# Kernel tuning notes

Measured on AMD Instinct MI355X. Metric: run time of the kernel, lower is better.

## Reference

```python
import jax, jax.numpy as jnp
import numpy as np

BS, IN, HID, LAT, OUT = 8192, 48, 256, 64, 128
CAT = LAT + OUT + HID  # LSTM input size = 448


def setup_inputs() -> dict:
    key = jax.random.key(0)
    ks = jax.random.split(key, 13)
    s = 0.02
    return {
        "x": jax.random.normal(ks[0], (BS, IN), jnp.float32),
        "enc": jax.random.normal(ks[1], (BS, HID), jnp.float32),
        "z": jax.random.normal(ks[2], (BS, LAT), jnp.float32),
        "W_ih": jax.random.normal(ks[3], (4 * OUT, CAT), jnp.float32) * s,
        "W_hh": jax.random.normal(ks[4], (4 * OUT, OUT), jnp.float32) * s,
        "b_ih": jax.random.normal(ks[5], (4 * OUT,), jnp.float32) * s,
        "b_hh": jax.random.normal(ks[6], (4 * OUT,), jnp.float32) * s,
        "W_u0": jax.random.normal(ks[7], (OUT, IN), jnp.float32) * s,
        "b_u0": jax.random.normal(ks[8], (OUT,), jnp.float32) * s,
        "W_h1": jax.random.normal(ks[9], (OUT, CAT), jnp.float32) * s,
        "b_h1": jax.random.normal(ks[10], (OUT,), jnp.float32) * s,
        "W_h2": jax.random.normal(ks[11], (OUT, CAT), jnp.float32) * s,
        "b_h2": jax.random.normal(ks[12], (OUT,), jnp.float32) * s,
        "horizon": 50,
    }


def reference(x, enc, z, W_ih, W_hh, b_ih, b_hh, W_u0, b_u0, W_h1, b_h1, W_h2, b_h2, horizon):
    # initial input u0 = Linear(input_size -> output_size)(x)
    u0 = x @ W_u0.T + b_u0                       # [bs, OUT]
    xi0 = jnp.concatenate([z, u0, enc], axis=-1)  # [bs, CAT]
    h0 = xi0 @ W_h1.T + b_h1                     # LSTM hidden init [bs, OUT]
    c0 = xi0 @ W_h2.T + b_h2                     # LSTM cell init   [bs, OUT]
    b = b_ih + b_hh

    def step(carry, _):
        h, c, yi = carry
        xi = jnp.concatenate([z, yi, enc], axis=-1)   # [bs, CAT]
        gates = xi @ W_ih.T + h @ W_hh.T + b          # [bs, 4*OUT]
        i_g, f_g, g_g, o_g = jnp.split(gates, 4, axis=-1)  # torch order: i,f,g,o
        c_new = jax.nn.sigmoid(f_g) * c + jax.nn.sigmoid(i_g) * jnp.tanh(g_g)
        h_new = jax.nn.sigmoid(o_g) * jnp.tanh(c_new)
        return (h_new, c_new, h_new), h_new

    _, ys = jax.lax.scan(step, (h0, c0, u0), None, length=horizon)  # [T, bs, OUT]
    # torch stacks yi [bs, 1, OUT] along dim=1 -> [bs, T, 1, OUT]
    return jnp.transpose(ys, (1, 0, 2))[:, :, None, :]
```

## Files before the change

### kernel.cpp

```cpp
#include <hip/hip_runtime.h>
#include <stdint.h>

typedef short bf16x8 __attribute__((ext_vector_type(8)));
typedef float f32x4 __attribute__((ext_vector_type(4)));

#define MFMA16(a,b,c) __builtin_amdgcn_mfma_f32_16x16x32_bf16((a),(b),(c),0,0,0)

__device__ __forceinline__ unsigned short bf16_rne(float f){
  unsigned int u = __builtin_bit_cast(unsigned int, f);
  return (unsigned short)((u + 0x7FFFu + ((u>>16)&1u)) >> 16);
}
__device__ __forceinline__ float bf16_f(unsigned short h){
  unsigned int u = ((unsigned int)h) << 16;
  return __builtin_bit_cast(float, u);
}

#define SZ_WINIT (48*24*512*2)
#define OFF_W0   (SZ_WINIT)
#define SZ_W0    (32*12*512*2)
#define OFF_WC   (OFF_W0 + SZ_W0)
#define SZ_WC    (32*8*512*2)
#define OFF_BIAS (OFF_WC + SZ_WC)

__device__ __forceinline__ void pack_split(unsigned short* __restrict__ base, int KT, int n, int k, float v){
  int nt = n>>4, n16 = n&15, kt = k>>5, kr = k&31;
  int lane = n16 + ((kr>>3)<<4), j = kr&7;
  unsigned short hi = bf16_rne(v);
  unsigned short lo = bf16_rne(v - bf16_f(hi));
  base[((nt*2*KT + kt)*64 + lane)*8 + j] = hi;
  base[((nt*2*KT + KT + kt)*64 + lane)*8 + j] = lo;
}

__global__ void decoder_prep(const float* __restrict__ W_ih, const float* __restrict__ W_hh,
                             const float* __restrict__ b_ih, const float* __restrict__ b_hh,
                             const float* __restrict__ W_u0, const float* __restrict__ b_u0,
                             const float* __restrict__ W_h1, const float* __restrict__ b_h1,
                             const float* __restrict__ W_h2, const float* __restrict__ b_h2,
                             unsigned short* __restrict__ wsu, float* __restrict__ bias_out){
  int idx = blockIdx.x*256 + threadIdx.x;
  if (idx < 768*384) {
    int n = idx/384, k = idx - n*384;
    float v = 0.f;
    if (n < 256) {
      const float* W = (n<128) ? (W_h1 + n*448) : (W_h2 + (n-128)*448);
      if (k < 64) v = W[k];
      else if (k < 320) v = W[192 + k - 64];
      else if (k < 368) { float s = 0.f; int j = k-320;
        for (int c=0;c<128;++c) s += W[64+c]*W_u0[c*48+j];
        v = s; }
    } else {
      int m = n-256;
      if (k < 64) v = W_ih[m*448 + k];
      else if (k < 320) v = W_ih[m*448 + 192 + k - 64];
    }
    pack_split(wsu, 12, n, k, v);
    return;
  }
  idx -= 768*384;
  if (idx < 512*192) {
    int n = idx/192, k = idx - n*192;
    float v = 0.f;
    if (k < 48)      { float s=0.f; for (int c=0;c<128;++c) s += W_ih[n*448+64+c]*W_u0[c*48+k]; v = s; }
    else if (k == 48){ float s=0.f; for (int c=0;c<128;++c) s += W_ih[n*448+64+c]*b_u0[c];      v = s; }
    else if (k >= 64)  v = W_hh[n*128 + k - 64];
    pack_split(wsu + OFF_W0/2, 6, n, k, v);
    return;
  }
  idx -= 512*192;
  if (idx < 512*128) {
    int n = idx>>7, k = idx&127;
    float v = W_ih[n*448 + 64 + k] + W_hh[n*128 + k];
    pack_split(wsu + OFF_WC/2, 4, n, k, v);
    return;
  }
  idx -= 512*128;
  if (idx < 768) {
    float v;
    if (idx < 256) {
      const float* W  = (idx<128) ? (W_h1 + idx*448) : (W_h2 + (idx-128)*448);
      float s = (idx<128) ? b_h1[idx] : b_h2[idx-128];
      for (int c=0;c<128;++c) s += W[64+c]*b_u0[c];
      v = s;
    } else v = b_ih[idx-256] + b_hh[idx-256];
    bias_out[idx] = v;
  }
}


__global__ __launch_bounds__(512, 2)
void decoder_main(const float* __restrict__ x, const float* __restrict__ enc, const float* __restrict__ z,
                  const unsigned short* __restrict__ wsu, const float* __restrict__ bias_init,
                  const int* __restrict__ hz, float* __restrict__ out){
  extern __shared__ char smem[];
  unsigned short* a0_hi = (unsigned short*)(smem);
  unsigned short* a0_lo = (unsigned short*)(smem + 12800);
  unsigned short* xi_hi = (unsigned short*)(smem + 25600);
  unsigned short* xi_lo = (unsigned short*)(smem + 50688);
  unsigned short* hbh   = (unsigned short*)(smem + 25600);
  unsigned short* hbl   = (unsigned short*)(smem + 43008);
  float*          c0l   = (float*)(smem + 60416);

  const int tid = threadIdx.x;
  const int w = tid>>6, lane = tid&63, n16 = lane&15, p = lane>>4;
  const int R0 = blockIdx.x*32;
  const int T = hz[0];

  for (int i = tid; i < 32*384; i += 512) {
    int r = i/384, c = i - r*384;
    float v;
    if (c < 64)       v = z[(R0+r)*64 + c];
    else if (c < 320) v = enc[(R0+r)*256 + c - 64];
    else if (c < 368) v = x[(R0+r)*48 + c - 320];
    else              v = 0.f;
    unsigned short hi = bf16_rne(v);
    xi_hi[r*392 + c] = hi;
    xi_lo[r*392 + c] = bf16_rne(v - bf16_f(hi));
  }
  for (int i = tid; i < 32*64; i += 512) {
    int r = i>>6, c = i&63;
    float v = (c<48) ? x[(R0+r)*48 + c] : (c==48 ? 1.f : 0.f);
    unsigned short hi = bf16_rne(v);
    a0_hi[r*200 + c] = hi;
    a0_lo[r*200 + c] = bf16_rne(v - bf16_f(hi));
  }
  __syncthreads();

  const bf16x8* WIp = (const bf16x8*)wsu;
  f32x4 accs[6][2];
  #pragma unroll
  for (int i=0;i<6;++i){
    int nt = (i<2) ? (2*w+i) : (16 + 8*(i-2) + w);
    float b = bias_init[nt*16 + n16];
    accs[i][0] = (f32x4){b,b,b,b};
    accs[i][1] = accs[i][0];
  }
  for (int kt=0; kt<12; ++kt) {
    bf16x8 ah0 = *(const bf16x8*)(xi_hi +      n16 *392 + kt*32 + p*8);
    bf16x8 ah1 = *(const bf16x8*)(xi_hi + (16+n16)*392 + kt*32 + p*8);
    bf16x8 al0 = *(const bf16x8*)(xi_lo +      n16 *392 + kt*32 + p*8);
    bf16x8 al1 = *(const bf16x8*)(xi_lo + (16+n16)*392 + kt*32 + p*8);
    #pragma unroll
    for (int i=0;i<6;++i){
      int nt = (i<2) ? (2*w+i) : (16 + 8*(i-2) + w);
      const bf16x8* fp = WIp + ((unsigned)(nt*24 + kt))*64 + lane;
      bf16x8 bh = fp[0];
      bf16x8 bl = fp[12*64];
      accs[i][0] = MFMA16(ah0, bh, accs[i][0]);
      accs[i][1] = MFMA16(ah1, bh, accs[i][1]);
      accs[i][0] = MFMA16(al0, bh, accs[i][0]);
      accs[i][1] = MFMA16(al1, bh, accs[i][1]);
      accs[i][0] = MFMA16(ah0, bl, accs[i][0]);
      accs[i][1] = MFMA16(ah1, bl, accs[i][1]);
    }
  }
  __syncthreads();

  #pragma unroll
  for (int i=0;i<2;++i){
    int ntg = 2*w + i;
    #pragma unroll
    for (int mt=0;mt<2;++mt){
      #pragma unroll
      for (int e=0;e<4;++e){
        int row = mt*16 + p*4 + e;
        float v = accs[i][mt][e];
        if (ntg < 8) {
          int col = 64 + ntg*16 + n16;
          unsigned short hi = bf16_rne(v);
          a0_hi[row*200 + col] = hi;
          a0_lo[row*200 + col] = bf16_rne(v - bf16_f(hi));
        } else {
          c0l[row*128 + (ntg-8)*16 + n16] = v;
        }
      }
    }
  }
  __syncthreads();

  f32x4 creg[2];
  #pragma unroll
  for (int mt=0;mt<2;++mt)
    #pragma unroll
    for (int e=0;e<4;++e)
      creg[mt][e] = c0l[(mt*16 + p*4 + e)*128 + w*16 + n16];

  f32x4 base_r[2][4];
  #pragma unroll
  for (int q=0;q<4;++q)
    #pragma unroll
    for (int mt=0;mt<2;++mt)
      base_r[mt][q] = accs[2+q][mt];

  const bf16x8* WCp = (const bf16x8*)(wsu + OFF_WC/2);
  bf16x8 wchi[4][4], wclo[4][4];
  #pragma unroll
  for (int q=0;q<4;++q){
    int nt = 8*q + w;
    #pragma unroll
    for (int kt=0;kt<4;++kt){
      wchi[q][kt] = WCp[((unsigned)(nt*8 + kt))*64 + lane];
      wclo[q][kt] = WCp[((unsigned)(nt*8 + 4 + kt))*64 + lane];
    }
  }

  unsigned rt[2][4];
  #pragma unroll
  for (int mt=0;mt<2;++mt)
    #pragma unroll
    for (int e=0;e<4;++e)
      rt[mt][e] = (unsigned)(R0 + mt*16 + p*4 + e)*(unsigned)(T*128) + (unsigned)(w*16 + n16);

  f32x4 acc[2][4];
  const float K1 = 1.44269504088896340736f;
  const float K2 = 2.88539008177792681472f;

  auto lstm_tail = [&](int t, int wb){
    #pragma unroll
    for (int mt=0;mt<2;++mt){
      #pragma unroll
      for (int e=0;e<4;++e){
        float iv = acc[mt][0][e], fv = acc[mt][1][e], gv = acc[mt][2][e], ov = acc[mt][3][e];
        float c = creg[mt][e];
        float ef = __builtin_amdgcn_exp2f(-K1*fv);
        float sf = __builtin_amdgcn_rcpf(1.f + ef);
        float ei = __builtin_amdgcn_exp2f(-K1*iv);
        float eg = __builtin_amdgcn_exp2f(-K2*gv);
        float d  = __builtin_amdgcn_rcpf((1.f+ei)*(1.f+eg));
        c = sf*c + (1.f-eg)*d;
        float eo = __builtin_amdgcn_exp2f(-K1*ov);
        float ec = __builtin_amdgcn_exp2f(-K2*c);
        float h  = (1.f-ec)*__builtin_amdgcn_rcpf((1.f+eo)*(1.f+ec));
        creg[mt][e] = c;
        out[rt[mt][e] + (unsigned)(t*128)] = h;
        int row = mt*16 + p*4 + e;
        unsigned short hh = bf16_rne(h);
        hbh[wb*4352 + row*136 + w*16 + n16] = hh;
        hbl[wb*4352 + row*136 + w*16 + n16] = bf16_rne(h - bf16_f(hh));
      }
    }
  };

  {
    const bf16x8* W0p = (const bf16x8*)(wsu + OFF_W0/2);
    #pragma unroll
    for (int kt=0;kt<6;++kt){
      bf16x8 ah0 = *(const bf16x8*)(a0_hi +      n16 *200 + kt*32 + p*8);
      bf16x8 ah1 = *(const bf16x8*)(a0_hi + (16+n16)*200 + kt*32 + p*8);
      bf16x8 al0 = *(const bf16x8*)(a0_lo +      n16 *200 + kt*32 + p*8);
      bf16x8 al1 = *(const bf16x8*)(a0_lo + (16+n16)*200 + kt*32 + p*8);
      #pragma unroll
      for (int q=0;q<4;++q){
        const bf16x8* fp = W0p + ((unsigned)((8*q+w)*12 + kt))*64 + lane;
        bf16x8 bh = fp[0];
        bf16x8 bl = fp[6*64];
        #pragma unroll
        for (int mt=0;mt<2;++mt){
          bf16x8 ah = mt ? ah1 : ah0;
          bf16x8 al = mt ? al1 : al0;
          f32x4 ci = (kt==0) ? base_r[mt][q] : acc[mt][q];
          ci = MFMA16(ah, bh, ci);
          ci = MFMA16(al, bh, ci);
          ci = MFMA16(ah, bl, ci);
          acc[mt][q] = ci;
        }
      }
    }
    lstm_tail(0, 0);
  }
  __syncthreads();

  for (int t=1; t<T; ++t){
    const int rb = (t-1)&1, wb = t&1;
    const unsigned short* hr = hbh + rb*4352;
    const unsigned short* lr = hbl + rb*4352;
    #pragma unroll
    for (int kt=0;kt<4;++kt){
      bf16x8 ah0 = *(const bf16x8*)(hr +      n16 *136 + kt*32 + p*8);
      bf16x8 ah1 = *(const bf16x8*)(hr + (16+n16)*136 + kt*32 + p*8);
      bf16x8 al0 = *(const bf16x8*)(lr +      n16 *136 + kt*32 + p*8);
      bf16x8 al1 = *(const bf16x8*)(lr + (16+n16)*136 + kt*32 + p*8);
      #pragma unroll
      for (int q=0;q<4;++q){
        #pragma unroll
        for (int mt=0;mt<2;++mt){
          bf16x8 ah = mt ? ah1 : ah0;
          bf16x8 al = mt ? al1 : al0;
          f32x4 ci = (kt==0) ? base_r[mt][q] : acc[mt][q];
          ci = MFMA16(ah, wchi[q][kt], ci);
          ci = MFMA16(al, wchi[q][kt], ci);
          ci = MFMA16(ah, wclo[q][kt], ci);
          acc[mt][q] = ci;
        }
      }
    }
    lstm_tail(t, wb);
    __syncthreads();
  }
}

extern "C" void kernel_launch(void* const* d_in, const int* in_sizes, int n_in,
                              void* d_out, int out_size, void* d_ws, size_t ws_size,
                              hipStream_t stream) {
    (void)in_sizes; (void)n_in; (void)out_size; (void)ws_size;
    const float* x    = (const float*)d_in[0];
    const float* enc  = (const float*)d_in[1];
    const float* z    = (const float*)d_in[2];
    const float* W_ih = (const float*)d_in[3];
    const float* W_hh = (const float*)d_in[4];
    const float* b_ih = (const float*)d_in[5];
    const float* b_hh = (const float*)d_in[6];
    const float* W_u0 = (const float*)d_in[7];
    const float* b_u0 = (const float*)d_in[8];
    const float* W_h1 = (const float*)d_in[9];
    const float* b_h1 = (const float*)d_in[10];
    const float* W_h2 = (const float*)d_in[11];
    const float* b_h2 = (const float*)d_in[12];
    const int*   hz   = (const int*)d_in[13];
    float* out = (float*)d_out;
    unsigned short* wsu = (unsigned short*)d_ws;
    float* bias = (float*)((char*)d_ws + OFF_BIAS);

    (void)hipFuncSetAttribute((const void*)decoder_main,
                              hipFuncAttributeMaxDynamicSharedMemorySize, 76800);

    decoder_prep<<<dim3(1795), dim3(256), 0, stream>>>(W_ih, W_hh, b_ih, b_hh, W_u0, b_u0,
                                                       W_h1, b_h1, W_h2, b_h2, wsu, bias);
    decoder_main<<<dim3(256), dim3(512), 76800, stream>>>(x, enc, z, wsu, bias, hz, out);
}
```

Before: 380.0 us.

## Rewrite weight prep into compose+pack kernels and swizzle LDS in decoder

Splits the weight preparation into a kernel that computes the W_u0 compositions once per row block using shared memory, and a pack kernel that writes full 8-element bf16 vectors per lane instead of scattered scalars. The main kernel swaps MFMA operand roles so the weights become the A operand, which lets the init results stay in registers (c0 and h0 written directly, no LDS round-trip for c0). It also adds XOR-swizzled LDS layouts to avoid bank conflicts, skips zero-padded k-tiles for the recurrent gate slices in the init GEMM, and emits vectorized f32x4 output stores one step later. This is many changes at once: it touches the prep cost, the LDS traffic, and the global store pattern, and the new index math carries some risk of errors.

```diff
diff --git a/kernel.cpp b/kernel.cpp
--- a/kernel.cpp
+++ b/kernel.cpp
@@ -3,6 +3,7 @@
 
 typedef short bf16x8 __attribute__((ext_vector_type(8)));
 typedef float f32x4 __attribute__((ext_vector_type(4)));
+typedef unsigned short u16x4 __attribute__((ext_vector_type(4)));
 
 #define MFMA16(a,b,c) __builtin_amdgcn_mfma_f32_16x16x32_bf16((a),(b),(c),0,0,0)
 
@@ -21,206 +22,240 @@
 #define OFF_WC   (OFF_W0 + SZ_W0)
 #define SZ_WC    (32*8*512*2)
 #define OFF_BIAS (OFF_WC + SZ_WC)
-
-__device__ __forceinline__ void pack_split(unsigned short* __restrict__ base, int KT, int n, int k, float v){
-  int nt = n>>4, n16 = n&15, kt = k>>5, kr = k&31;
-  int lane = n16 + ((kr>>3)<<4), j = kr&7;
-  unsigned short hi = bf16_rne(v);
-  unsigned short lo = bf16_rne(v - bf16_f(hi));
-  base[((nt*2*KT + kt)*64 + lane)*8 + j] = hi;
-  base[((nt*2*KT + KT + kt)*64 + lane)*8 + j] = lo;
-}
-
-__global__ void decoder_prep(const float* __restrict__ W_ih, const float* __restrict__ W_hh,
-                             const float* __restrict__ b_ih, const float* __restrict__ b_hh,
-                             const float* __restrict__ W_u0, const float* __restrict__ b_u0,
-                             const float* __restrict__ W_h1, const float* __restrict__ b_h1,
-                             const float* __restrict__ W_h2, const float* __restrict__ b_h2,
-                             unsigned short* __restrict__ wsu, float* __restrict__ bias_out){
-  int idx = blockIdx.x*256 + threadIdx.x;
-  if (idx < 768*384) {
-    int n = idx/384, k = idx - n*384;
-    float v = 0.f;
-    if (n < 256) {
-      const float* W = (n<128) ? (W_h1 + n*448) : (W_h2 + (n-128)*448);
-      if (k < 64) v = W[k];
-      else if (k < 320) v = W[192 + k - 64];
-      else if (k < 368) { float s = 0.f; int j = k-320;
-        for (int c=0;c<128;++c) s += W[64+c]*W_u0[c*48+j];
-        v = s; }
-    } else {
-      int m = n-256;
-      if (k < 64) v = W_ih[m*448 + k];
-      else if (k < 320) v = W_ih[m*448 + 192 + k - 64];
-    }
-    pack_split(wsu, 12, n, k, v);
+#define OFF_XQ   (OFF_BIAS + 4096)
+#define OFF_XH   (OFF_XQ + 512*49*4)
+
+__global__ __launch_bounds__(256)
+void decoder_compose(const float* __restrict__ W_ih, const float* __restrict__ W_u0,
+                     const float* __restrict__ b_u0, const float* __restrict__ W_h1,
+                     const float* __restrict__ W_h2, float* __restrict__ ws){
+  __shared__ float wu[128][49];
+  __shared__ float wrow[16][128];
+  float* Xq = (float*)((char*)ws + OFF_XQ);
+  float* Xh = (float*)((char*)ws + OFF_XH);
+  const int b = blockIdx.x, tid = threadIdx.x;
+  for (int i = tid; i < 128*49; i += 256){
+    int c = i/49, j = i - c*49;
+    wu[c][j] = (j < 48) ? W_u0[c*48 + j] : b_u0[c];
+  }
+  for (int i = tid; i < 16*128; i += 256){
+    int r = i>>7, c = i&127;
+    const float* src;
+    if (b < 32) src = W_ih + (b*16 + r)*448 + 64;
+    else { int mm = (b-32)*16 + r; src = (mm<128) ? (W_h1 + mm*448 + 64) : (W_h2 + (mm-128)*448 + 64); }
+    wrow[r][c] = src[c];
+  }
+  __syncthreads();
+  for (int o = tid; o < 16*49; o += 256){
+    int r = o/49, j = o - r*49;
+    float s = 0.f;
+    #pragma unroll 8
+    for (int c = 0; c < 128; ++c) s += wrow[r][c]*wu[c][j];
+    if (b < 32) Xq[(b*16+r)*49 + j] = s;
+    else        Xh[((b-32)*16+r)*49 + j] = s;
+  }
+}
+
+__global__ __launch_bounds__(256)
+void decoder_pack(const float* __restrict__ W_ih, const float* __restrict__ W_hh,
+                  const float* __restrict__ b_ih, const float* __restrict__ b_hh,
+                  const float* __restrict__ W_h1, const float* __restrict__ W_h2,
+                  const float* __restrict__ b_h1, const float* __restrict__ b_h2,
+                  unsigned short* __restrict__ wsu, float* __restrict__ ws){
+  const float* Xq = (const float*)((const char*)ws + OFF_XQ);
+  const float* Xh = (const float*)((const char*)ws + OFF_XH);
+  float* bias = (float*)((char*)ws + OFF_BIAS);
+  const int gid = blockIdx.x*256 + threadIdx.x;
+  const int slot = gid >> 6, lane = gid & 63;
+  const int n16 = lane & 15, p = lane >> 4;
+
+  float v[8];
+  unsigned short* dh; unsigned short* dl;
+  if (slot < 576) {
+    int nt = slot/12, kt = slot - nt*12;
+    int n = nt*16 + n16;
+    #pragma unroll
+    for (int j=0;j<8;++j){
+      int k = kt*32 + p*8 + j;
+      float xv = 0.f;
+      if (n < 256) {
+        const float* W = (n<128) ? (W_h1 + n*448) : (W_h2 + (n-128)*448);
+        if (k < 64) xv = W[k];
+        else if (k < 320) xv = W[192 + k - 64];
+        else if (k < 368) xv = Xh[n*49 + (k-320)];
+      } else {
+        int m = n - 256;
+        if (k < 64) xv = W_ih[m*448 + k];
+        else if (k < 320) xv = W_ih[m*448 + 192 + k - 64];
+      }
+      v[j] = xv;
+    }
+    dh = wsu + ((nt*24 + kt)*64 + lane)*8;
+    dl = wsu + ((nt*24 + 12 + kt)*64 + lane)*8;
+  } else if (slot < 768) {
+    int s2 = slot - 576;
+    int nt = s2/6, kt = s2 - nt*6;
+    int n = nt*16 + n16;
+    #pragma unroll
+    for (int j=0;j<8;++j){
+      int k = kt*32 + p*8 + j;
+      float xv = 0.f;
+      if (k < 49)      xv = Xq[n*49 + k];
+      else if (k >= 64) xv = W_hh[n*128 + k - 64];
+      v[j] = xv;
+    }
+    unsigned short* b = wsu + OFF_W0/2;
+    dh = b + ((nt*12 + kt)*64 + lane)*8;
+    dl = b + ((nt*12 + 6 + kt)*64 + lane)*8;
+  } else if (slot < 896) {
+    int s3 = slot - 768;
+    int nt = s3>>2, kt = s3&3;
+    int n = nt*16 + n16;
+    #pragma unroll
+    for (int j=0;j<8;++j){
+      int k = kt*32 + p*8 + j;
+      v[j] = W_ih[n*448 + 64 + k] + W_hh[n*128 + k];
+    }
+    unsigned short* b = wsu + OFF_WC/2;
+    dh = b + ((nt*8 + kt)*64 + lane)*8;
+    dl = b + ((nt*8 + 4 + kt)*64 + lane)*8;
+  } else {
+    int i = gid - 896*64;
+    if (i < 768) {
+      float bv;
+      if (i < 128)      bv = b_h1[i] + Xh[i*49 + 48];
+      else if (i < 256) bv = b_h2[i-128] + Xh[i*49 + 48];
+      else              bv = b_ih[i-256] + b_hh[i-256];
+      bias[i] = bv;
+    }
     return;
   }
-  idx -= 768*384;
-  if (idx < 512*192) {
-    int n = idx/192, k = idx - n*192;
-    float v = 0.f;
-    if (k < 48)      { float s=0.f; for (int c=0;c<128;++c) s += W_ih[n*448+64+c]*W_u0[c*48+k]; v = s; }
-    else if (k == 48){ float s=0.f; for (int c=0;c<128;++c) s += W_ih[n*448+64+c]*b_u0[c];      v = s; }
-    else if (k >= 64)  v = W_hh[n*128 + k - 64];
-    pack_split(wsu + OFF_W0/2, 6, n, k, v);
-    return;
-  }
-  idx -= 512*192;
-  if (idx < 512*128) {
-    int n = idx>>7, k = idx&127;
-    float v = W_ih[n*448 + 64 + k] + W_hh[n*128 + k];
-    pack_split(wsu + OFF_WC/2, 4, n, k, v);
-    return;
-  }
-  idx -= 512*128;
-  if (idx < 768) {
-    float v;
-    if (idx < 256) {
-      const float* W  = (idx<128) ? (W_h1 + idx*448) : (W_h2 + (idx-128)*448);
-      float s = (idx<128) ? b_h1[idx] : b_h2[idx-128];
-      for (int c=0;c<128;++c) s += W[64+c]*b_u0[c];
-      v = s;
-    } else v = b_ih[idx-256] + b_hh[idx-256];
-    bias_out[idx] = v;
-  }
-}
-
+  bf16x8 vh, vl;
+  #pragma unroll
+  for (int j=0;j<8;++j){
+    unsigned short h = bf16_rne(v[j]);
+    vh[j] = (short)h;
+    vl[j] = (short)bf16_rne(v[j] - bf16_f(h));
+  }
+  *(bf16x8*)dh = vh;
+  *(bf16x8*)dl = vl;
+}
+
+#define LDS_A0H 0
+#define LDS_A0L 12288
+#define LDS_XIH 24576
+#define LDS_XIL 49152
+#define LDS_H   24576
+#define LDS_TOTAL 73728
 
 __global__ __launch_bounds__(512, 2)
 void decoder_main(const float* __restrict__ x, const float* __restrict__ enc, const float* __restrict__ z,
-                  const unsigned short* __restrict__ wsu, const float* __restrict__ bias_init,
+                  const unsigned short* __restrict__ wsu, const float* __restrict__ bias,
                   const int* __restrict__ hz, float* __restrict__ out){
   extern __shared__ char smem[];
-  unsigned short* a0_hi = (unsigned short*)(smem);
-  unsigned short* a0_lo = (unsigned short*)(smem + 12800);
-  unsigned short* xi_hi = (unsigned short*)(smem + 25600);
-  unsigned short* xi_lo = (unsigned short*)(smem + 50688);
-  unsigned short* hbh   = (unsigned short*)(smem + 25600);
-  unsigned short* hbl   = (unsigned short*)(smem + 43008);
-  float*          c0l   = (float*)(smem + 60416);
-
   const int tid = threadIdx.x;
   const int w = tid>>6, lane = tid&63, n16 = lane&15, p = lane>>4;
+  const int p16 = p*16;
   const int R0 = blockIdx.x*32;
   const int T = hz[0];
 
-  for (int i = tid; i < 32*384; i += 512) {
+  for (int i = tid; i < 32*384; i += 512){
     int r = i/384, c = i - r*384;
     float v;
     if (c < 64)       v = z[(R0+r)*64 + c];
     else if (c < 320) v = enc[(R0+r)*256 + c - 64];
     else if (c < 368) v = x[(R0+r)*48 + c - 320];
     else              v = 0.f;
-    unsigned short hi = bf16_rne(v);
-    xi_hi[r*392 + c] = hi;
-    xi_lo[r*392 + c] = bf16_rne(v - bf16_f(hi));
-  }
-  for (int i = tid; i < 32*64; i += 512) {
+    unsigned short h = bf16_rne(v);
+    int off = r*768 + ((2*c) ^ ((r&7)<<4));
+    *(unsigned short*)(smem + LDS_XIH + off) = h;
+    *(unsigned short*)(smem + LDS_XIL + off) = bf16_rne(v - bf16_f(h));
+  }
+  for (int i = tid; i < 32*64; i += 512){
     int r = i>>6, c = i&63;
-    float v = (c<48) ? x[(R0+r)*48 + c] : (c==48 ? 1.f : 0.f);
-    unsigned short hi = bf16_rne(v);
-    a0_hi[r*200 + c] = hi;
-    a0_lo[r*200 + c] = bf16_rne(v - bf16_f(hi));
-  }
-  __syncthreads();
-
-  const bf16x8* WIp = (const bf16x8*)wsu;
+    float v = (c < 48) ? x[(R0+r)*48 + c] : (c == 48 ? 1.f : 0.f);
+    unsigned short h = bf16_rne(v);
+    int off = r*384 + ((2*c) ^ ((r&7)<<4));
+    *(unsigned short*)(smem + LDS_A0H + off) = h;
+    *(unsigned short*)(smem + LDS_A0L + off) = bf16_rne(v - bf16_f(h));
+  }
+  __syncthreads();
+
+  const int row0 = n16, row1 = 16 + n16;
+  const int s0 = (row0&7)<<4, s1 = (row1&7)<<4;
+
   f32x4 accs[6][2];
   #pragma unroll
   for (int i=0;i<6;++i){
-    int nt = (i<2) ? (2*w+i) : (16 + 8*(i-2) + w);
-    float b = bias_init[nt*16 + n16];
-    accs[i][0] = (f32x4){b,b,b,b};
-    accs[i][1] = accs[i][0];
-  }
-  for (int kt=0; kt<12; ++kt) {
-    bf16x8 ah0 = *(const bf16x8*)(xi_hi +      n16 *392 + kt*32 + p*8);
-    bf16x8 ah1 = *(const bf16x8*)(xi_hi + (16+n16)*392 + kt*32 + p*8);
-    bf16x8 al0 = *(const bf16x8*)(xi_lo +      n16 *392 + kt*32 + p*8);
-    bf16x8 al1 = *(const bf16x8*)(xi_lo + (16+n16)*392 + kt*32 + p*8);
+    int nt = (i==0) ? w : (i==1) ? (8+w) : (16 + 8*(i-2) + w);
+    f32x4 bv = *(const f32x4*)(bias + nt*16 + p*4);
+    accs[i][0] = bv; accs[i][1] = bv;
+  }
+  #pragma unroll
+  for (int kt=0; kt<12; ++kt){
+    bf16x8 bh0 = *(const bf16x8*)(smem + LDS_XIH + row0*768 + ((kt*64 + p16) ^ s0));
+    bf16x8 bh1 = *(const bf16x8*)(smem + LDS_XIH + row1*768 + ((kt*64 + p16) ^ s1));
+    bf16x8 bl0 = *(const bf16x8*)(smem + LDS_XIL + row0*768 + ((kt*64 + p16) ^ s0));
+    bf16x8 bl1 = *(const bf16x8*)(smem + LDS_XIL + row1*768 + ((kt*64 + p16) ^ s1));
+    bf16x8 wa[6], wl[6];
     #pragma unroll
     for (int i=0;i<6;++i){
-      int nt = (i<2) ? (2*w+i) : (16 + 8*(i-2) + w);
-      const bf16x8* fp = WIp + ((unsigned)(nt*24 + kt))*64 + lane;
-      bf16x8 bh = fp[0];
-      bf16x8 bl = fp[12*64];
-      accs[i][0] = MFMA16(ah0, bh, accs[i][0]);
-      accs[i][1] = MFMA16(ah1, bh, accs[i][1]);
-      accs[i][0] = MFMA16(al0, bh, accs[i][0]);
-      accs[i][1] = MFMA16(al1, bh, accs[i][1]);
-      accs[i][0] = MFMA16(ah0, bl, accs[i][0]);
-      accs[i][1] = MFMA16(ah1, bl, accs[i][1]);
-    }
-  }
-  __syncthreads();
-
-  #pragma unroll
-  for (int i=0;i<2;++i){
-    int ntg = 2*w + i;
-    #pragma unroll
-    for (int mt=0;mt<2;++mt){
-      #pragma unroll
-      for (int e=0;e<4;++e){
-        int row = mt*16 + p*4 + e;
-        float v = accs[i][mt][e];
-        if (ntg < 8) {
-          int col = 64 + ntg*16 + n16;
-          unsigned short hi = bf16_rne(v);
-          a0_hi[row*200 + col] = hi;
-          a0_lo[row*200 + col] = bf16_rne(v - bf16_f(hi));
-        } else {
-          c0l[row*128 + (ntg-8)*16 + n16] = v;
-        }
-      }
-    }
-  }
-  __syncthreads();
-
-  f32x4 creg[2];
-  #pragma unroll
-  for (int mt=0;mt<2;++mt)
-    #pragma unroll
-    for (int e=0;e<4;++e)
-      creg[mt][e] = c0l[(mt*16 + p*4 + e)*128 + w*16 + n16];
-
+      if (kt >= 10 && i >= 2) continue;
+      int nt = (i==0) ? w : (i==1) ? (8+w) : (16 + 8*(i-2) + w);
+      wa[i] = *(const bf16x8*)(wsu + ((nt*24 + kt)*64 + lane)*8);
+      wl[i] = *(const bf16x8*)(wsu + ((nt*24 + 12 + kt)*64 + lane)*8);
+    }
+    #pragma unroll
+    for (int i=0;i<6;++i){ if (kt >= 10 && i >= 2) continue;
+      accs[i][0] = MFMA16(wa[i], bh0, accs[i][0]);
+      accs[i][1] = MFMA16(wa[i], bh1, accs[i][1]); }
+    #pragma unroll
+    for (int i=0;i<6;++i){ if (kt >= 10 && i >= 2) continue;
+      accs[i][0] = MFMA16(wa[i], bl0, accs[i][0]);
+      accs[i][1] = MFMA16(wa[i], bl1, accs[i][1]); }
+    #pragma unroll
+    for (int i=0;i<6;++i){ if (kt >= 10 && i >= 2) continue;
+      accs[i][0] = MFMA16(wl[i], bh0, accs[i][0]);
+      accs[i][1] = MFMA16(wl[i], bh1, accs[i][1]); }
+  }
+  __syncthreads();
+
+  #pragma unroll
+  for (int bt=0; bt<2; ++bt){
+    int row = bt*16 + n16, s = (row&7)<<4;
+    u16x4 vh, vl;
+    #pragma unroll
+    for (int e=0;e<4;++e){
+      float hv = accs[0][bt][e];
+      unsigned short h = bf16_rne(hv);
+      vh[e] = h; vl[e] = bf16_rne(hv - bf16_f(h));
+    }
+    int off = row*384 + ((128 + 32*w + 8*p) ^ s);
+    *(u16x4*)(smem + LDS_A0H + off) = vh;
+    *(u16x4*)(smem + LDS_A0L + off) = vl;
+  }
+  f32x4 creg[2] = { accs[1][0], accs[1][1] };
   f32x4 base_r[2][4];
   #pragma unroll
-  for (int q=0;q<4;++q)
-    #pragma unroll
-    for (int mt=0;mt<2;++mt)
-      base_r[mt][q] = accs[2+q][mt];
-
-  const bf16x8* WCp = (const bf16x8*)(wsu + OFF_WC/2);
-  bf16x8 wchi[4][4], wclo[4][4];
-  #pragma unroll
-  for (int q=0;q<4;++q){
-    int nt = 8*q + w;
-    #pragma unroll
-    for (int kt=0;kt<4;++kt){
-      wchi[q][kt] = WCp[((unsigned)(nt*8 + kt))*64 + lane];
-      wclo[q][kt] = WCp[((unsigned)(nt*8 + 4 + kt))*64 + lane];
-    }
-  }
-
-  unsigned rt[2][4];
-  #pragma unroll
-  for (int mt=0;mt<2;++mt)
-    #pragma unroll
-    for (int e=0;e<4;++e)
-      rt[mt][e] = (unsigned)(R0 + mt*16 + p*4 + e)*(unsigned)(T*128) + (unsigned)(w*16 + n16);
+  for (int q=0;q<4;++q){ base_r[0][q] = accs[2+q][0]; base_r[1][q] = accs[2+q][1]; }
+  __syncthreads();
+
+  float* outp0 = out + (size_t)(R0 + n16)      * (size_t)(T*128) + (16*w + 4*p);
+  float* outp1 = out + (size_t)(R0 + 16 + n16) * (size_t)(T*128) + (16*w + 4*p);
 
   f32x4 acc[2][4];
+  f32x4 hcur0, hcur1;
   const float K1 = 1.44269504088896340736f;
   const float K2 = 2.88539008177792681472f;
 
-  auto lstm_tail = [&](int t, int wb){
-    #pragma unroll
-    for (int mt=0;mt<2;++mt){
+  auto lstm_tail = [&](int wb){
+    #pragma unroll
+    for (int bt=0; bt<2; ++bt){
+      f32x4 hh;
       #pragma unroll
       for (int e=0;e<4;++e){
-        float iv = acc[mt][0][e], fv = acc[mt][1][e], gv = acc[mt][2][e], ov = acc[mt][3][e];
-        float c = creg[mt][e];
+        float iv = acc[bt][0][e], fv = acc[bt][1][e], gv = acc[bt][2][e], ov = acc[bt][3][e];
+        float c = creg[bt][e];
         float ef = __builtin_amdgcn_exp2f(-K1*fv);
         float sf = __builtin_amdgcn_rcpf(1.f + ef);
         float ei = __builtin_amdgcn_exp2f(-K1*iv);
@@ -230,72 +265,103 @@
         float eo = __builtin_amdgcn_exp2f(-K1*ov);
         float ec = __builtin_amdgcn_exp2f(-K2*c);
         float h  = (1.f-ec)*__builtin_amdgcn_rcpf((1.f+eo)*(1.f+ec));
-        creg[mt][e] = c;
-        out[rt[mt][e] + (unsigned)(t*128)] = h;
-        int row = mt*16 + p*4 + e;
-        unsigned short hh = bf16_rne(h);
-        hbh[wb*4352 + row*136 + w*16 + n16] = hh;
-        hbl[wb*4352 + row*136 + w*16 + n16] = bf16_rne(h - bf16_f(hh));
-      }
+        creg[bt][e] = c; hh[e] = h;
+      }
+      if (bt == 0) hcur0 = hh; else hcur1 = hh;
+      int row = bt*16 + n16, s = (row&7)<<4;
+      u16x4 ph, pl;
+      #pragma unroll
+      for (int e=0;e<4;++e){
+        unsigned short h = bf16_rne(hh[e]);
+        ph[e] = h; pl[e] = bf16_rne(hh[e] - bf16_f(h));
+      }
+      int off = row*256 + ((32*w + 8*p) ^ s);
+      *(u16x4*)(smem + LDS_H + (wb*2+0)*8192 + off) = ph;
+      *(u16x4*)(smem + LDS_H + (wb*2+1)*8192 + off) = pl;
     }
   };
 
   {
-    const bf16x8* W0p = (const bf16x8*)(wsu + OFF_W0/2);
-    #pragma unroll
-    for (int kt=0;kt<6;++kt){
-      bf16x8 ah0 = *(const bf16x8*)(a0_hi +      n16 *200 + kt*32 + p*8);
-      bf16x8 ah1 = *(const bf16x8*)(a0_hi + (16+n16)*200 + kt*32 + p*8);
-      bf16x8 al0 = *(const bf16x8*)(a0_lo +      n16 *200 + kt*32 + p*8);
-      bf16x8 al1 = *(const bf16x8*)(a0_lo + (16+n16)*200 + kt*32 + p*8);
-      #pragma unroll
-      for (int q=0;q<4;++q){
-        const bf16x8* fp = W0p + ((unsigned)((8*q+w)*12 + kt))*64 + lane;
-        bf16x8 bh = fp[0];
-        bf16x8 bl = fp[6*64];
-        #pragma unroll
-        for (int mt=0;mt<2;++mt){
-          bf16x8 ah = mt ? ah1 : ah0;
-          bf16x8 al = mt ? al1 : al0;
-          f32x4 ci = (kt==0) ? base_r[mt][q] : acc[mt][q];
-          ci = MFMA16(ah, bh, ci);
-          ci = MFMA16(al, bh, ci);
-          ci = MFMA16(ah, bl, ci);
-          acc[mt][q] = ci;
-        }
-      }
-    }
-    lstm_tail(0, 0);
+    const unsigned short* W0p = wsu + OFF_W0/2;
+    #pragma unroll
+    for (int kt=0; kt<6; ++kt){
+      bf16x8 bh0 = *(const bf16x8*)(smem + LDS_A0H + row0*384 + ((kt*64 + p16) ^ s0));
+      bf16x8 bh1 = *(const bf16x8*)(smem + LDS_A0H + row1*384 + ((kt*64 + p16) ^ s1));
+      bf16x8 bl0 = *(const bf16x8*)(smem + LDS_A0L + row0*384 + ((kt*64 + p16) ^ s0));
+      bf16x8 bl1 = *(const bf16x8*)(smem + LDS_A0L + row1*384 + ((kt*64 + p16) ^ s1));
+      bf16x8 wa[4], wl[4];
+      #pragma unroll
+      for (int q=0;q<4;++q){
+        wa[q] = *(const bf16x8*)(W0p + (((8*q+w)*12 + kt)*64 + lane)*8);
+        wl[q] = *(const bf16x8*)(W0p + (((8*q+w)*12 + 6 + kt)*64 + lane)*8);
+      }
+      #pragma unroll
+      for (int q=0;q<4;++q){
+        f32x4 c0i = kt ? acc[0][q] : base_r[0][q];
+        f32x4 c1i = kt ? acc[1][q] : base_r[1][q];
+        acc[0][q] = MFMA16(wa[q], bh0, c0i);
+        acc[1][q] = MFMA16(wa[q], bh1, c1i);
+      }
+      #pragma unroll
+      for (int q=0;q<4;++q){
+        acc[0][q] = MFMA16(wa[q], bl0, acc[0][q]);
+        acc[1][q] = MFMA16(wa[q], bl1, acc[1][q]);
+      }
+      #pragma unroll
+      for (int q=0;q<4;++q){
+        acc[0][q] = MFMA16(wl[q], bh0, acc[0][q]);
+        acc[1][q] = MFMA16(wl[q], bh1, acc[1][q]);
+      }
+    }
+    lstm_tail(0);
+  }
+
+  const unsigned short* WCp = wsu + OFF_WC/2;
+  bf16x8 wchi[4][4], wclo[4][4];
+  #pragma unroll
+  for (int q=0;q<4;++q){
+    #pragma unroll
+    for (int kt=0;kt<4;++kt){
+      wchi[q][kt] = *(const bf16x8*)(WCp + (((8*q+w)*8 + kt)*64 + lane)*8);
+      wclo[q][kt] = *(const bf16x8*)(WCp + (((8*q+w)*8 + 4 + kt)*64 + lane)*8);
+    }
   }
   __syncthreads();
 
   for (int t=1; t<T; ++t){
+    *(f32x4*)(outp0 + (t-1)*128) = hcur0;
+    *(f32x4*)(outp1 + (t-1)*128) = hcur1;
     const int rb = (t-1)&1, wb = t&1;
-    const unsigned short* hr = hbh + rb*4352;
-    const unsigned short* lr = hbl + rb*4352;
-    #pragma unroll
-    for (int kt=0;kt<4;++kt){
-      bf16x8 ah0 = *(const bf16x8*)(hr +      n16 *136 + kt*32 + p*8);
-      bf16x8 ah1 = *(const bf16x8*)(hr + (16+n16)*136 + kt*32 + p*8);
-      bf16x8 al0 = *(const bf16x8*)(lr +      n16 *136 + kt*32 + p*8);
-      bf16x8 al1 = *(const bf16x8*)(lr + (16+n16)*136 + kt*32 + p*8);
-      #pragma unroll
-      for (int q=0;q<4;++q){
-        #pragma unroll
-        for (int mt=0;mt<2;++mt){
-          bf16x8 ah = mt ? ah1 : ah0;
-          bf16x8 al = mt ? al1 : al0;
-          f32x4 ci = (kt==0) ? base_r[mt][q] : acc[mt][q];
-          ci = MFMA16(ah, wchi[q][kt], ci);
-          ci = MFMA16(al, wchi[q][kt], ci);
-          ci = MFMA16(ah, wclo[q][kt], ci);
-          acc[mt][q] = ci;
-        }
-      }
-    }
-    lstm_tail(t, wb);
+    const char* hb = smem + LDS_H + rb*2*8192;
+    #pragma unroll
+    for (int kt=0; kt<4; ++kt){
+      bf16x8 bh0 = *(const bf16x8*)(hb + row0*256 + ((kt*64 + p16) ^ s0));
+      bf16x8 bh1 = *(const bf16x8*)(hb + row1*256 + ((kt*64 + p16) ^ s1));
+      bf16x8 bl0 = *(const bf16x8*)(hb + 8192 + row0*256 + ((kt*64 + p16) ^ s0));
+      bf16x8 bl1 = *(const bf16x8*)(hb + 8192 + row1*256 + ((kt*64 + p16) ^ s1));
+      #pragma unroll
+      for (int q=0;q<4;++q){
+        f32x4 c0i = kt ? acc[0][q] : base_r[0][q];
+        f32x4 c1i = kt ? acc[1][q] : base_r[1][q];
+        acc[0][q] = MFMA16(wchi[q][kt], bh0, c0i);
+        acc[1][q] = MFMA16(wchi[q][kt], bh1, c1i);
+      }
+      #pragma unroll
+      for (int q=0;q<4;++q){
+        acc[0][q] = MFMA16(wchi[q][kt], bl0, acc[0][q]);
+        acc[1][q] = MFMA16(wchi[q][kt], bl1, acc[1][q]);
+      }
+      #pragma unroll
+      for (int q=0;q<4;++q){
+        acc[0][q] = MFMA16(wclo[q][kt], bh0, acc[0][q]);
+        acc[1][q] = MFMA16(wclo[q][kt], bh1, acc[1][q]);
+      }
+    }
+    lstm_tail(wb);
     __syncthreads();
   }
+  *(f32x4*)(outp0 + (T-1)*128) = hcur0;
+  *(f32x4*)(outp1 + (T-1)*128) = hcur1;
 }
 
 extern "C" void kernel_launch(void* const* d_in, const int* in_sizes, int n_in,
@@ -319,11 +385,13 @@
     float* out = (float*)d_out;
     unsigned short* wsu = (unsigned short*)d_ws;
     float* bias = (float*)((char*)d_ws + OFF_BIAS);
+    float* wsf  = (float*)d_ws;
 
     (void)hipFuncSetAttribute((const void*)decoder_main,
-                              hipFuncAttributeMaxDynamicSharedMemorySize, 76800);
-
-    decoder_prep<<<dim3(1795), dim3(256), 0, stream>>>(W_ih, W_hh, b_ih, b_hh, W_u0, b_u0,
-                                                       W_h1, b_h1, W_h2, b_h2, wsu, bias);
-    decoder_main<<<dim3(256), dim3(512), 76800, stream>>>(x, enc, z, wsu, bias, hz, out);
-}
+                              hipFuncAttributeMaxDynamicSharedMemorySize, LDS_TOTAL);
+
+    decoder_compose<<<dim3(48), dim3(256), 0, stream>>>(W_ih, W_u0, b_u0, W_h1, W_h2, wsf);
+    decoder_pack<<<dim3(227), dim3(256), 0, stream>>>(W_ih, W_hh, b_ih, b_hh,
+                                                      W_h1, W_h2, b_h1, b_h2, wsu, wsf);
+    decoder_main<<<dim3(256), dim3(512), LDS_TOTAL, stream>>>(x, enc, z, wsu, bias, hz, out);
+}
```

Result: no change. 374.9 us (-1.4%).
